# Kernel tuning notes

Hardware: AMD Instinct MI355X
Metric: run time of the kernel (lower is better)

## Reference

```python
import jax, jax.numpy as jnp
import numpy as np

B, S, DIM, H = 2, 2048, 2048, 16
HD = DIM // H  # head_dim = 128
EPS = 1e-6


def setup_inputs() -> dict:
    key = jax.random.key(0)
    ks = jax.random.split(key, 13)
    d = {
        'hidden_states': jax.random.normal(ks[0], (B, S, DIM), jnp.float32),
        'freqs_cos': jax.random.normal(ks[1], (1, S, 1, HD), jnp.float32),
        'freqs_sin': jax.random.normal(ks[2], (1, S, 1, HD), jnp.float32),
        'Wq': jax.random.normal(ks[3], (DIM, DIM), jnp.float32) * 0.02,
        'bq': jax.random.normal(ks[4], (DIM,), jnp.float32) * 0.02,
        'Wk': jax.random.normal(ks[5], (DIM, DIM), jnp.float32) * 0.02,
        'bk': jax.random.normal(ks[6], (DIM,), jnp.float32) * 0.02,
        'Wv': jax.random.normal(ks[7], (DIM, DIM), jnp.float32) * 0.02,
        'bv': jax.random.normal(ks[8], (DIM,), jnp.float32) * 0.02,
        'norm_q_w': jax.random.uniform(ks[9], (DIM,), jnp.float32, 0.5, 1.5),
        'norm_k_w': jax.random.uniform(ks[10], (DIM,), jnp.float32, 0.5, 1.5),
        'Wo': jax.random.normal(ks[11], (DIM, DIM), jnp.float32) * 0.02,
        'bo': jax.random.normal(ks[12], (DIM,), jnp.float32) * 0.02,
    }
    return d


def _rms_norm(x, w, eps=EPS):
    # local RMSNorm over the full inner_dim (no cross-rank reduce)
    xf = x.astype(jnp.float32)
    var = jnp.mean(xf * xf, axis=-1, keepdims=True)
    return (w * (xf * jax.lax.rsqrt(var + eps))).astype(x.dtype)


def _apply_rope(x, freqs_cos, freqs_sin):
    # x: [B,H,S,D]; freqs: [1,S,1,D] -> broadcast cos/sin at [1,1,S,D/2]
    dtype = x.dtype
    xf = x.astype(jnp.float32)
    x1 = xf[..., 0::2]
    x2 = xf[..., 1::2]
    cos = jnp.transpose(freqs_cos[..., 0::2], (0, 2, 1, 3)).astype(jnp.float32)
    sin = jnp.transpose(freqs_sin[..., 1::2], (0, 2, 1, 3)).astype(jnp.float32)
    even = x1 * cos - x2 * sin
    odd = x1 * sin + x2 * cos
    out = jnp.stack([even, odd], axis=-1).reshape(x.shape)
    return out.astype(dtype)


def reference(hidden_states, freqs_cos, freqs_sin, Wq, bq, Wk, bk, Wv, bv,
              norm_q_w, norm_k_w, Wo, bo):
    b, s, _ = hidden_states.shape
    q = hidden_states @ Wq.T + bq
    k = hidden_states @ Wk.T + bk
    v = hidden_states @ Wv.T + bv
    q = _rms_norm(q, norm_q_w)
    k = _rms_norm(k, norm_k_w)
    # [B,S,H*D] -> [B,H,S,D]
    q = q.reshape(b, s, H, HD).transpose(0, 2, 1, 3)
    k = k.reshape(b, s, H, HD).transpose(0, 2, 1, 3)
    v = v.reshape(b, s, H, HD).transpose(0, 2, 1, 3)
    q = _apply_rope(q, freqs_cos, freqs_sin)
    k = _apply_rope(k, freqs_cos, freqs_sin)
    # flash attention math (full, non-causal), scale = 1/sqrt(head_dim)
    scale = 1.0 / np.sqrt(HD).astype(np.float32)
    scores = jnp.einsum('bhqd,bhkd->bhqk', q, k) * scale
    attn = jax.nn.softmax(scores, axis=-1)
    out = jnp.einsum('bhqk,bhkd->bhqd', attn, v)
    out = out.transpose(0, 2, 1, 3).reshape(b, s, H * HD)
    return out @ Wo.T + bo
```

## Files before the change

kernel.cpp:

```cpp
#include <hip/hip_runtime.h>
#include <stdint.h>

#define DEVI __device__ __forceinline__

typedef __attribute__((ext_vector_type(8))) short bf16x8;
typedef __attribute__((ext_vector_type(4))) float f32x4;
typedef __attribute__((ext_vector_type(16))) float f32x16;
typedef __attribute__((ext_vector_type(4))) unsigned short u16x4;
typedef __attribute__((ext_vector_type(8))) unsigned short u16x8;

DEVI unsigned short f2bf(float f) {
    union { float f; unsigned u; } v; v.f = f;
    unsigned r = v.u + 0x7fffu + ((v.u >> 16) & 1u);
    return (unsigned short)(r >> 16);
}

DEVI float bf2f(unsigned short u) {
    union { unsigned u; float f; } v; v.u = ((unsigned)u) << 16;
    return v.f;
}

DEVI unsigned cvtpk(float lo, float hi) {
    unsigned r;
    asm("v_cvt_pk_bf16_f32 %0, %1, %2" : "=v"(r) : "v"(lo), "v"(hi));
    return r;
}

DEVI void gload16(const void* g, void* lds) {
    __builtin_amdgcn_global_load_lds(
        (const __attribute__((address_space(1))) unsigned int*)(uintptr_t)g,
        (__attribute__((address_space(3))) unsigned int*)(unsigned int)(uintptr_t)lds,
        16, 0, 0);
}

__global__ __launch_bounds__(256) void cvt_all(
    const float* __restrict__ hs, const float* __restrict__ wq,
    const float* __restrict__ wk, const float* __restrict__ wv,
    const float* __restrict__ wo,
    unsigned short* __restrict__ o_hs, unsigned short* __restrict__ o_wq,
    unsigned short* __restrict__ o_wk, unsigned short* __restrict__ o_wv,
    unsigned short* __restrict__ o_wo) {
    const int bid = blockIdx.x;
    const float* src; unsigned short* dst; int base;
    if (bid < 2048)      { src = hs; dst = o_hs; base = bid; }
    else if (bid < 3072) { src = wq; dst = o_wq; base = bid - 2048; }
    else if (bid < 4096) { src = wk; dst = o_wk; base = bid - 3072; }
    else if (bid < 5120) { src = wv; dst = o_wv; base = bid - 4096; }
    else                 { src = wo; dst = o_wo; base = bid - 5120; }
    const int i0 = base * 1024 + threadIdx.x;
#pragma unroll
    for (int k = 0; k < 4; k++) {
        const int i = i0 + k * 256;
        float4 v = ((const float4*)src)[i];
        u16x4 pk;
        pk[0] = f2bf(v.x); pk[1] = f2bf(v.y); pk[2] = f2bf(v.z); pk[3] = f2bf(v.w);
        ((u16x4*)dst)[i] = pk;
    }
}

DEVI void gemm_core256(const unsigned short* __restrict__ A,
                       const unsigned short* __restrict__ Wt,
                       int m0, int n0, char* lds,
                       f32x4 (&acc)[8][4]) {
    constexpr int K = 2048;
    const int t = threadIdx.x;
    const int w = t >> 6, l = t & 63, lr = l & 15, lk = l >> 4;
    const int wr = w >> 2, wc = w & 3;
    const int sx = lr & 7;
    const int srow = t >> 3, sseg = (t & 7) ^ (srow & 7);
    const unsigned short* aS = A + (size_t)(m0 + srow) * K + sseg * 8;
    const unsigned short* bS = Wt + (size_t)(n0 + srow) * K + sseg * 8;

#pragma unroll
    for (int mi = 0; mi < 8; mi++)
#pragma unroll
        for (int ni = 0; ni < 4; ni++) acc[mi][ni] = (f32x4){0.f, 0.f, 0.f, 0.f};

    auto STAGE = [&](int tt, int u) {
        if (tt >= 32) return;
        const int k0 = tt * 64, bb = tt & 1;
        if (u < 4)
            gload16(aS + (size_t)u * 64 * K + k0, lds + bb * 32768 + u * 8192 + w * 1024);
        else
            gload16(bS + (size_t)(u - 4) * 64 * K + k0,
                    lds + 65536 + bb * 32768 + (u - 4) * 8192 + w * 1024);
    };

    STAGE(0, 0); STAGE(0, 1); STAGE(0, 2); STAGE(0, 3);
    STAGE(0, 4); STAGE(0, 5); STAGE(0, 6); STAGE(0, 7);
    STAGE(1, 0); STAGE(1, 1); STAGE(1, 2); STAGE(1, 3);
    asm volatile("s_waitcnt vmcnt(4)" ::: "memory");
    __builtin_amdgcn_s_barrier();

    for (int kt = 0; kt < 32; ++kt) {
        const int bb = kt & 1;
        const char* Ab = lds + bb * 32768;
        const char* Bb = lds + 65536 + bb * 32768;
        bf16x8 a[8][2], b[4][2];
#pragma unroll
        for (int mi = 0; mi < 8; mi++)
#pragma unroll
            for (int ks = 0; ks < 2; ks++)
                a[mi][ks] = *(const bf16x8*)(Ab + (wr * 128 + mi * 16 + lr) * 128 +
                                             (((ks * 4 + lk) ^ sx) << 4));
#pragma unroll
        for (int ni = 0; ni < 4; ni++)
#pragma unroll
            for (int ks = 0; ks < 2; ks++)
                b[ni][ks] = *(const bf16x8*)(Bb + (wc * 64 + ni * 16 + lr) * 128 +
                                             (((ks * 4 + lk) ^ sx) << 4));
        STAGE(kt + 1, 4); STAGE(kt + 1, 5); STAGE(kt + 1, 6); STAGE(kt + 1, 7);
        __builtin_amdgcn_s_setprio(1);
#pragma unroll
        for (int mi = 0; mi < 8; mi++)
#pragma unroll
            for (int ni = 0; ni < 4; ni++)
                acc[mi][ni] = __builtin_amdgcn_mfma_f32_16x16x32_bf16(
                    a[mi][0], b[ni][0], acc[mi][ni], 0, 0, 0);
        __builtin_amdgcn_s_setprio(0);
        asm volatile("s_waitcnt lgkmcnt(0)" ::: "memory");
        __builtin_amdgcn_s_barrier();
        STAGE(kt + 2, 0); STAGE(kt + 2, 1); STAGE(kt + 2, 2); STAGE(kt + 2, 3);
        __builtin_amdgcn_s_setprio(1);
#pragma unroll
        for (int mi = 0; mi < 8; mi++)
#pragma unroll
            for (int ni = 0; ni < 4; ni++)
                acc[mi][ni] = __builtin_amdgcn_mfma_f32_16x16x32_bf16(
                    a[mi][1], b[ni][1], acc[mi][ni], 0, 0, 0);
        __builtin_amdgcn_s_setprio(0);
        if (kt < 30)       asm volatile("s_waitcnt vmcnt(4)" ::: "memory");
        else if (kt == 30) asm volatile("s_waitcnt vmcnt(0)" ::: "memory");
        __builtin_amdgcn_s_barrier();
    }
}

DEVI void gemm_pipe_core(const unsigned short* __restrict__ A,
                         const unsigned short* __restrict__ Wt,
                         int m0, int n0, char* lds,
                         f32x4 (&acc)[2][2][2][2]) {
    constexpr int K = 2048;
    const int t = threadIdx.x;
    const int w = t >> 6, l = t & 63, lr = l & 15, lk = l >> 4;
    const int wr = w >> 2, wc = w & 3;
    const int sx = lr & 7;
    const int srow = t >> 3, sseg = (t & 7) ^ (srow & 7);
    const unsigned short* aS = A + (size_t)(m0 + srow) * K + sseg * 8;
    const unsigned short* bS = Wt + (size_t)(n0 + srow) * K + sseg * 8;
    char* Bbase = lds + 32768;

#pragma unroll
    for (int qm = 0; qm < 2; qm++)
#pragma unroll
        for (int qn = 0; qn < 2; qn++)
#pragma unroll
            for (int fr = 0; fr < 2; fr++)
#pragma unroll
                for (int fc = 0; fc < 2; fc++)
                    acc[qm][qn][fr][fc] = (f32x4){0.f, 0.f, 0.f, 0.f};

    auto STAGE = [&](int tt, int u) {
        if (tt >= 32) return;
        const int k0 = tt * 64, bb = tt & 1;
        if (u < 4)
            gload16(bS + (size_t)u * 64 * K + k0, Bbase + bb * 32768 + u * 8192 + w * 1024);
        else
            gload16(aS + (size_t)(u - 4) * 64 * K + k0, lds + bb * 16384 + (u - 4) * 8192 + w * 1024);
    };

    STAGE(0, 0); STAGE(0, 1); STAGE(0, 2); STAGE(0, 3); STAGE(0, 4); STAGE(0, 5);
    STAGE(1, 0); STAGE(1, 1); STAGE(1, 2);
    asm volatile("s_waitcnt vmcnt(3)" ::: "memory");
    __builtin_amdgcn_s_barrier();

    for (int kt = 0; kt < 32; ++kt) {
        const int bb = kt & 1;
        const char* Ab = lds + bb * 16384;
        const char* Bb = Bbase + bb * 32768;
        bf16x8 a0[2][2], a1[2][2], b0[2][2], b1[2][2];
#pragma unroll
        for (int fr = 0; fr < 2; fr++)
#pragma unroll
            for (int ks = 0; ks < 2; ks++) {
                a0[fr][ks] = *(const bf16x8*)(Ab + (wr * 64 + fr * 16 + lr) * 128 +
                                              (((ks * 4 + lk) ^ sx) << 4));
                a1[fr][ks] = *(const bf16x8*)(Ab + (wr * 64 + 32 + fr * 16 + lr) * 128 +
                                              (((ks * 4 + lk) ^ sx) << 4));
            }
#pragma unroll
        for (int fc = 0; fc < 2; fc++)
#pragma unroll
            for (int ks = 0; ks < 2; ks++) {
                b0[fc][ks] = *(const bf16x8*)(Bb + (wc * 64 + fc * 16 + lr) * 128 +
                                              (((ks * 4 + lk) ^ sx) << 4));
                b1[fc][ks] = *(const bf16x8*)(Bb + (wc * 64 + 32 + fc * 16 + lr) * 128 +
                                              (((ks * 4 + lk) ^ sx) << 4));
            }
        STAGE(kt + 1, 3); STAGE(kt + 1, 4); STAGE(kt + 1, 5);
        __builtin_amdgcn_s_setprio(1);
#pragma unroll
        for (int ks = 0; ks < 2; ks++)
#pragma unroll
            for (int fr = 0; fr < 2; fr++)
#pragma unroll
                for (int fc = 0; fc < 2; fc++) {
                    acc[0][0][fr][fc] = __builtin_amdgcn_mfma_f32_16x16x32_bf16(
                        a0[fr][ks], b0[fc][ks], acc[0][0][fr][fc], 0, 0, 0);
                    acc[1][0][fr][fc] = __builtin_amdgcn_mfma_f32_16x16x32_bf16(
                        a1[fr][ks], b0[fc][ks], acc[1][0][fr][fc], 0, 0, 0);
                }
        __builtin_amdgcn_s_setprio(0);
        asm volatile("s_waitcnt lgkmcnt(0)" ::: "memory");
        __builtin_amdgcn_s_barrier();
        STAGE(kt + 2, 0); STAGE(kt + 2, 1); STAGE(kt + 2, 2);
        __builtin_amdgcn_s_setprio(1);
#pragma unroll
        for (int ks = 0; ks < 2; ks++)
#pragma unroll
            for (int fr = 0; fr < 2; fr++)
#pragma unroll
                for (int fc = 0; fc < 2; fc++) {
                    acc[0][1][fr][fc] = __builtin_amdgcn_mfma_f32_16x16x32_bf16(
                        a0[fr][ks], b1[fc][ks], acc[0][1][fr][fc], 0, 0, 0);
                    acc[1][1][fr][fc] = __builtin_amdgcn_mfma_f32_16x16x32_bf16(
                        a1[fr][ks], b1[fc][ks], acc[1][1][fr][fc], 0, 0, 0);
                }
        __builtin_amdgcn_s_setprio(0);
        if (kt < 30)       asm volatile("s_waitcnt vmcnt(3)" ::: "memory");
        else if (kt == 30) asm volatile("s_waitcnt vmcnt(0)" ::: "memory");
        __builtin_amdgcn_s_barrier();
    }
}

__global__ __launch_bounds__(512, 2) void gemm_qkv(
    const unsigned short* __restrict__ A,
    const unsigned short* __restrict__ Wq16, const unsigned short* __restrict__ Wk16,
    const unsigned short* __restrict__ Wv16,
    const float* __restrict__ bq, const float* __restrict__ bk, const float* __restrict__ bv,
    unsigned short* __restrict__ qh, unsigned short* __restrict__ kh,
    unsigned short* __restrict__ Vt) {
    __shared__ char Lds[131072];
    const int bid = blockIdx.x;
    const int nt = bid & 7, idx = bid >> 3;
    const int mt = idx & 15, z = idx >> 4;
    const int m0 = mt * 256, n0 = nt * 256;
    const unsigned short* W = (z == 0) ? Wq16 : (z == 1) ? Wk16 : Wv16;
    const float* bias = (z == 0) ? bq : (z == 1) ? bk : bv;

    f32x4 acc[8][4];
    gemm_core256(A, W, m0, n0, Lds, acc);

    const int t = threadIdx.x, w = t >> 6, l = t & 63, lr = l & 15, lk = l >> 4;
    const int wr = w >> 2, wc = w & 3;
#pragma unroll
    for (int mi = 0; mi < 8; mi++)
#pragma unroll
        for (int ni = 0; ni < 4; ni++) {
            const int col = n0 + wc * 64 + ni * 16 + lr;
            const int rb = m0 + wr * 128 + mi * 16 + lk * 4;
            const float bb = bias[col];
            if (z == 2) {
                const int hh = col >> 7, d = col & 127;
                const int b = rb >> 11, s = rb & 2047;
                u16x4 pk;
#pragma unroll
                for (int j = 0; j < 4; j++) pk[j] = f2bf(acc[mi][ni][j] + bb);
                *(u16x4*)(Vt + ((size_t)((b * 16 + hh) * 128 + d)) * 2048 + s) = pk;
            } else {
                unsigned short* out = (z == 0) ? qh : kh;
#pragma unroll
                for (int j = 0; j < 4; j++)
                    out[(size_t)(rb + j) * 2048 + col] = f2bf(acc[mi][ni][j] + bb);
            }
        }
}

__global__ __launch_bounds__(512, 2) void gemm_o(
    const unsigned short* __restrict__ A, const unsigned short* __restrict__ W16,
    const float* __restrict__ bo, float* __restrict__ out) {
    __shared__ char Lds[98304];
    const int bid = blockIdx.x;
    const int nt = bid & 7, mt = bid >> 3;
    const int m0 = mt * 128, n0 = nt * 256;

    f32x4 acc[2][2][2][2];
    gemm_pipe_core(A, W16, m0, n0, Lds, acc);

    const int t = threadIdx.x, w = t >> 6, l = t & 63, lr = l & 15, lk = l >> 4;
    const int wr = w >> 2, wc = w & 3;
#pragma unroll
    for (int qm = 0; qm < 2; qm++)
#pragma unroll
        for (int qn = 0; qn < 2; qn++)
#pragma unroll
            for (int fr = 0; fr < 2; fr++)
#pragma unroll
                for (int fc = 0; fc < 2; fc++) {
                    const int col = n0 + wc * 64 + qn * 32 + fc * 16 + lr;
                    const int rb = m0 + wr * 64 + qm * 32 + fr * 16 + lk * 4;
                    const float bb = bo[col];
#pragma unroll
                    for (int j = 0; j < 4; j++)
                        out[(size_t)(rb + j) * 2048 + col] = acc[qm][qn][fr][fc][j] + bb;
                }
}

__global__ __launch_bounds__(256) void norm_rope(
    const unsigned short* __restrict__ qh, const unsigned short* __restrict__ kh,
    const float* __restrict__ nqw, const float* __restrict__ nkw,
    const float* __restrict__ fc, const float* __restrict__ fs,
    unsigned short* __restrict__ Qr, unsigned short* __restrict__ Kr) {
    const int row = blockIdx.x;
    const int which = blockIdx.y;
    const unsigned short* in = which ? kh : qh;
    const float* wv = which ? nkw : nqw;
    unsigned short* out = which ? Kr : Qr;
    const float qs = which ? 1.0f : 0.12751744f;
    const int t = threadIdx.x;
    u16x8 xr = *(const u16x8*)(in + (size_t)row * 2048 + t * 8);
    float xv[8];
#pragma unroll
    for (int e = 0; e < 8; e++) xv[e] = bf2f(xr[e]);
    float ss = 0.f;
#pragma unroll
    for (int e = 0; e < 8; e++) ss += xv[e] * xv[e];
#pragma unroll
    for (int m = 1; m < 64; m <<= 1) ss += __shfl_xor(ss, m, 64);
    __shared__ float red[4];
    if ((t & 63) == 0) red[t >> 6] = ss;
    __syncthreads();
    const float tot = red[0] + red[1] + red[2] + red[3];
    const float r = rsqrtf(tot * (1.0f / 2048.0f) + 1e-6f);
    const int s = row & 2047, b = row >> 11;
    const int d0 = t * 8, hd0 = d0 & 127, h = d0 >> 7;
    float4 c0 = ((const float4*)(fc + s * 128 + hd0))[0];
    float4 c1 = ((const float4*)(fc + s * 128 + hd0))[1];
    float4 s0 = ((const float4*)(fs + s * 128 + hd0))[0];
    float4 s1 = ((const float4*)(fs + s * 128 + hd0))[1];
    float4 w0 = ((const float4*)(wv + d0))[0];
    float4 w1 = ((const float4*)(wv + d0))[1];
    float wn[8] = {w0.x, w0.y, w0.z, w0.w, w1.x, w1.y, w1.z, w1.w};
    float xn[8];
#pragma unroll
    for (int e = 0; e < 8; e++) xn[e] = xv[e] * wn[e] * r;
    float o[8];
    o[0] = xn[0] * c0.x - xn[1] * s0.y;  o[1] = xn[0] * s0.y + xn[1] * c0.x;
    o[2] = xn[2] * c0.z - xn[3] * s0.w;  o[3] = xn[2] * s0.w + xn[3] * c0.z;
    o[4] = xn[4] * c1.x - xn[5] * s1.y;  o[5] = xn[4] * s1.y + xn[5] * c1.x;
    o[6] = xn[6] * c1.z - xn[7] * s1.w;  o[7] = xn[6] * s1.w + xn[7] * c1.z;
    u16x8 pk;
#pragma unroll
    for (int e = 0; e < 8; e++) pk[e] = f2bf(o[e] * qs);
    *(u16x8*)(out + ((size_t)((b * 16 + h) * 2048 + s)) * 128 + hd0) = pk;
}

__global__ __launch_bounds__(256, 2) void attn(
    const unsigned short* __restrict__ Qr, const unsigned short* __restrict__ Kr,
    const unsigned short* __restrict__ Vt, unsigned short* __restrict__ Ao) {
    __shared__ unsigned short Kl[2][64 * 128];
    __shared__ unsigned short Vl[2][128 * 64];
    const int t = threadIdx.x, w = t >> 6, l = t & 63;
    const int ql = l & 31, h = l >> 5;
    const int bid = blockIdx.x;
    const int xcd = bid & 7, idx = bid >> 3;
    const int bh = xcd * 4 + (idx >> 4);
    const int q0 = (idx & 15) * 128 + w * 32;
    const int b = bh >> 4, head = bh & 15;

    const unsigned short* Qp = Qr + ((size_t)bh * 2048 + q0) * 128;
    bf16x8 qf[8];
#pragma unroll
    for (int c8 = 0; c8 < 8; c8++)
        qf[c8] = *(const bf16x8*)(Qp + ql * 128 + c8 * 16 + h * 8);

    f32x16 accO[4];
#pragma unroll
    for (int dt = 0; dt < 4; dt++)
#pragma unroll
        for (int r = 0; r < 16; r++) accO[dt][r] = 0.f;
    float mj = -1e30f, ljp = 0.f;

    const unsigned short* Kb = Kr + (size_t)bh * 2048 * 128;
    const unsigned short* Vb = Vt + (size_t)bh * 128 * 2048;
    const int krow = t >> 4, kseg = (t & 15) ^ (krow & 7);
    const int vrow = t >> 3, vseg = (t & 7) ^ (vrow & 7);

    auto STAGE = [&](int buf, int kv0) {
        char* kd = (char*)&Kl[buf][0] + w * 1024;
        char* vd = (char*)&Vl[buf][0] + w * 1024;
#pragma unroll
        for (int c = 0; c < 4; c++)
            gload16(Kb + (size_t)(kv0 + c * 16 + krow) * 128 + kseg * 8, kd + c * 4096);
#pragma unroll
        for (int c = 0; c < 4; c++)
            gload16(Vb + (size_t)(c * 32 + vrow) * 2048 + kv0 + vseg * 8, vd + c * 4096);
    };

    const int qx = ql & 7;
    STAGE(0, 0);
    __syncthreads();
    int cur = 0;
    for (int it = 0; it < 32; ++it) {
        if (it < 31) STAGE(cur ^ 1, (it + 1) * 64);
        f32x16 S0, S1;
#pragma unroll
        for (int r = 0; r < 16; r++) { S0[r] = 0.f; S1[r] = 0.f; }
        __builtin_amdgcn_s_setprio(1);
#pragma unroll
        for (int c8 = 0; c8 < 8; c8++) {
            const int sg = ((c8 * 2 + h) ^ qx) << 4;
            bf16x8 k0 = *(const bf16x8*)((const char*)&Kl[cur][0] + ql * 256 + sg);
            bf16x8 k1 = *(const bf16x8*)((const char*)&Kl[cur][0] + (32 + ql) * 256 + sg);
            S0 = __builtin_amdgcn_mfma_f32_32x32x16_bf16(k0, qf[c8], S0, 0, 0, 0);
            S1 = __builtin_amdgcn_mfma_f32_32x32x16_bf16(k1, qf[c8], S1, 0, 0, 0);
        }
        __builtin_amdgcn_s_setprio(0);
        float mloc = S0[0];
#pragma unroll
        for (int r = 1; r < 16; r++) mloc = fmaxf(mloc, S0[r]);
#pragma unroll
        for (int r = 0; r < 16; r++) mloc = fmaxf(mloc, S1[r]);
        const float mx = fmaxf(mloc, __shfl_xor(mloc, 32, 64));
        if (!__all(mx <= mj + 8.0f)) {
            const float mn = fmaxf(mj, mx);
            const float corr = exp2f(mj - mn);
            mj = mn;
            ljp *= corr;
#pragma unroll
            for (int dt = 0; dt < 4; dt++)
#pragma unroll
                for (int r = 0; r < 16; r++) accO[dt][r] *= corr;
        }
        unsigned W[16];
        float lsum = 0.f;
#pragma unroll
        for (int i = 0; i < 8; i++) {
            const float pa = exp2f(S0[2 * i] - mj);
            const float pb = exp2f(S0[2 * i + 1] - mj);
            W[i] = cvtpk(pa, pb);
            lsum += pa + pb;
        }
#pragma unroll
        for (int i = 0; i < 8; i++) {
            const float pa = exp2f(S1[2 * i] - mj);
            const float pb = exp2f(S1[2 * i + 1] - mj);
            W[8 + i] = cvtpk(pa, pb);
            lsum += pa + pb;
        }
        ljp += lsum;
#pragma unroll
        for (int c = 0; c < 2; c++) {
            unsigned X[8];
#pragma unroll
            for (int i = 0; i < 8; i++)
                X[i] = (unsigned)__shfl_xor((int)W[c * 8 + i], 32, 64);
            union U { unsigned u[4]; bf16x8 v; };
            U F, G;
            F.u[0] = h ? X[2] : W[c * 8 + 0];
            F.u[1] = h ? X[3] : W[c * 8 + 1];
            F.u[2] = h ? W[c * 8 + 2] : X[0];
            F.u[3] = h ? W[c * 8 + 3] : X[1];
            G.u[0] = h ? X[6] : W[c * 8 + 4];
            G.u[1] = h ? X[7] : W[c * 8 + 5];
            G.u[2] = h ? W[c * 8 + 6] : X[4];
            G.u[3] = h ? W[c * 8 + 7] : X[5];
            __builtin_amdgcn_s_setprio(1);
#pragma unroll
            for (int dt = 0; dt < 4; dt++) {
                const int sg = (((2 * c) * 2 + h) ^ qx) << 4;
                bf16x8 vf = *(const bf16x8*)((const char*)&Vl[cur][0] + (dt * 32 + ql) * 128 + sg);
                accO[dt] = __builtin_amdgcn_mfma_f32_32x32x16_bf16(vf, F.v, accO[dt], 0, 0, 0);
            }
#pragma unroll
            for (int dt = 0; dt < 4; dt++) {
                const int sg = (((2 * c + 1) * 2 + h) ^ qx) << 4;
                bf16x8 vf = *(const bf16x8*)((const char*)&Vl[cur][0] + (dt * 32 + ql) * 128 + sg);
                accO[dt] = __builtin_amdgcn_mfma_f32_32x32x16_bf16(vf, G.v, accO[dt], 0, 0, 0);
            }
            __builtin_amdgcn_s_setprio(0);
        }
        __syncthreads();
        cur ^= 1;
    }
    const float lj = ljp + __shfl_xor(ljp, 32, 64);
    const float inv = 1.0f / lj;
    unsigned short* ob = Ao + ((size_t)(b * 2048 + q0 + ql)) * 2048 + head * 128;
#pragma unroll
    for (int dt = 0; dt < 4; dt++)
#pragma unroll
        for (int i = 0; i < 8; i++) {
            const float a = accO[dt][2 * i] * inv;
            const float c = accO[dt][2 * i + 1] * inv;
            const int d = dt * 32 + ((2 * i) & 3) + 8 * (i >> 1) + 4 * h;
            *(unsigned*)(ob + d) = cvtpk(a, c);
        }
}

extern "C" void kernel_launch(void* const* d_in, const int* in_sizes, int n_in,
                              void* d_out, int out_size, void* d_ws, size_t ws_size,
                              hipStream_t stream) {
    const float* hs  = (const float*)d_in[0];
    const float* fc  = (const float*)d_in[1];
    const float* fs  = (const float*)d_in[2];
    const float* Wq  = (const float*)d_in[3];
    const float* bq  = (const float*)d_in[4];
    const float* Wk  = (const float*)d_in[5];
    const float* bk  = (const float*)d_in[6];
    const float* Wv  = (const float*)d_in[7];
    const float* bv  = (const float*)d_in[8];
    const float* nqw = (const float*)d_in[9];
    const float* nkw = (const float*)d_in[10];
    const float* Wo  = (const float*)d_in[11];
    const float* bo  = (const float*)d_in[12];
    float* out = (float*)d_out;

    char* p = (char*)d_ws;
    unsigned short* hs16 = (unsigned short*)p; p += (size_t)8388608 * 2;
    unsigned short* Wq16 = (unsigned short*)p; p += (size_t)4194304 * 2;
    unsigned short* Wk16 = (unsigned short*)p; p += (size_t)4194304 * 2;
    unsigned short* Wv16 = (unsigned short*)p; p += (size_t)4194304 * 2;
    unsigned short* Wo16 = (unsigned short*)p; p += (size_t)4194304 * 2;
    unsigned short* qh = (unsigned short*)p;   p += (size_t)8388608 * 2;
    unsigned short* kh = (unsigned short*)p;   p += (size_t)8388608 * 2;
    unsigned short* Qr = (unsigned short*)p;   p += (size_t)8388608 * 2;
    unsigned short* Kr = (unsigned short*)p;   p += (size_t)8388608 * 2;
    unsigned short* Vt = (unsigned short*)p;   p += (size_t)8388608 * 2;
    unsigned short* Ao = (unsigned short*)p;   p += (size_t)8388608 * 2;
    (void)ws_size; (void)in_sizes; (void)n_in; (void)out_size;

    cvt_all<<<6144, 256, 0, stream>>>(hs, Wq, Wk, Wv, Wo,
                                      hs16, Wq16, Wk16, Wv16, Wo16);
    gemm_qkv<<<384, 512, 0, stream>>>(hs16, Wq16, Wk16, Wv16,
                                      bq, bk, bv, qh, kh, Vt);
    norm_rope<<<dim3(4096, 2), 256, 0, stream>>>(qh, kh, nqw, nkw, fc, fs, Qr, Kr);
    attn<<<512, 256, 0, stream>>>(Qr, Kr, Vt, Ao);
    gemm_o<<<256, 512, 0, stream>>>(Ao, Wo16, bo, out);
}
```

Baseline: 298.5 us.

## Split QKV GEMM main loop into eight-phase interleaved load/MFMA schedule

Restructures the 256x256 QKV GEMM K-loop into four sub-phases per tile. Each phase loads a slice of A fragments, issues one half of the next A or B tile's global-to-LDS copies, and runs the matching MFMA block. B becomes the operand prefetched two tiles ahead instead of A. The goal is to overlap LDS reads, global prefetch and MFMA more finely and to hold fewer A fragments in registers. The cost is more barriers per tile, which adds synchronisation overhead and hazard risk.

New measurement: 304.4 us. Within noise of the previous version (+2.0%).

```diff
diff --git a/kernel.cpp b/kernel.cpp
--- a/kernel.cpp
+++ b/kernel.cpp
@@ -58,11 +58,11 @@
     }
 }
 
-DEVI void gemm_core256(const unsigned short* __restrict__ A,
-                       const unsigned short* __restrict__ Wt,
-                       int m0, int n0, char* lds,
-                       f32x4 (&acc)[8][4]) {
-    constexpr int K = 2048;
+DEVI void gemm_core256_8ph(const unsigned short* __restrict__ A,
+                           const unsigned short* __restrict__ Wt,
+                           int m0, int n0, char* lds,
+                           f32x4 (&acc)[8][4]) {
+    constexpr int K = 2048, NT = 32;
     const int t = threadIdx.x;
     const int w = t >> 6, l = t & 63, lr = l & 15, lk = l >> 4;
     const int wr = w >> 2, wc = w & 3;
@@ -76,62 +76,72 @@
 #pragma unroll
         for (int ni = 0; ni < 4; ni++) acc[mi][ni] = (f32x4){0.f, 0.f, 0.f, 0.f};
 
-    auto STAGE = [&](int tt, int u) {
-        if (tt >= 32) return;
+    auto STAGE_A = [&](int tt, int half) {
+        if (tt >= NT) return;
         const int k0 = tt * 64, bb = tt & 1;
-        if (u < 4)
-            gload16(aS + (size_t)u * 64 * K + k0, lds + bb * 32768 + u * 8192 + w * 1024);
-        else
-            gload16(bS + (size_t)(u - 4) * 64 * K + k0,
-                    lds + 65536 + bb * 32768 + (u - 4) * 8192 + w * 1024);
+        char* d = lds + bb * 32768 + half * 16384 + w * 1024;
+        gload16(aS + (size_t)(half * 128) * K + k0, d);
+        gload16(aS + (size_t)(half * 128 + 64) * K + k0, d + 8192);
     };
-
-    STAGE(0, 0); STAGE(0, 1); STAGE(0, 2); STAGE(0, 3);
-    STAGE(0, 4); STAGE(0, 5); STAGE(0, 6); STAGE(0, 7);
-    STAGE(1, 0); STAGE(1, 1); STAGE(1, 2); STAGE(1, 3);
+    auto STAGE_B = [&](int tt, int half) {
+        if (tt >= NT) return;
+        const int k0 = tt * 64, bb = tt & 1;
+        char* d = lds + 65536 + bb * 32768 + half * 16384 + w * 1024;
+        gload16(bS + (size_t)(half * 128) * K + k0, d);
+        gload16(bS + (size_t)(half * 128 + 64) * K + k0, d + 8192);
+    };
+
+    STAGE_A(0, 0); STAGE_A(0, 1);
+    STAGE_B(0, 0); STAGE_B(0, 1);
+    STAGE_B(1, 0); STAGE_B(1, 1);
     asm volatile("s_waitcnt vmcnt(4)" ::: "memory");
     __builtin_amdgcn_s_barrier();
 
-    for (int kt = 0; kt < 32; ++kt) {
+    for (int kt = 0; kt < NT; ++kt) {
         const int bb = kt & 1;
         const char* Ab = lds + bb * 32768;
         const char* Bb = lds + 65536 + bb * 32768;
-        bf16x8 a[8][2], b[4][2];
-#pragma unroll
-        for (int mi = 0; mi < 8; mi++)
+        bf16x8 b[4][2];
+#pragma unroll
+        for (int p = 0; p < 4; ++p) {
+            bf16x8 a[2][2];
+            if (p == 0) {
+#pragma unroll
+                for (int ni = 0; ni < 4; ni++)
+#pragma unroll
+                    for (int ks = 0; ks < 2; ks++)
+                        b[ni][ks] = *(const bf16x8*)(Bb + (wc * 64 + ni * 16 + lr) * 128 +
+                                                     (((ks * 4 + lk) ^ sx) << 4));
+            }
+#pragma unroll
+            for (int mi = 0; mi < 2; mi++)
+#pragma unroll
+                for (int ks = 0; ks < 2; ks++)
+                    a[mi][ks] = *(const bf16x8*)(Ab + (wr * 128 + (2 * p + mi) * 16 + lr) * 128 +
+                                                 (((ks * 4 + lk) ^ sx) << 4));
+            if (p == 0)      STAGE_A(kt + 1, 0);
+            else if (p == 1) STAGE_A(kt + 1, 1);
+            else if (p == 2) STAGE_B(kt + 2, 0);
+            else             STAGE_B(kt + 2, 1);
+            if (p == 0) asm volatile("s_waitcnt lgkmcnt(8)" ::: "memory");
+            __builtin_amdgcn_s_barrier();
+            asm volatile("s_waitcnt lgkmcnt(0)" ::: "memory");
+            __builtin_amdgcn_s_setprio(1);
 #pragma unroll
             for (int ks = 0; ks < 2; ks++)
-                a[mi][ks] = *(const bf16x8*)(Ab + (wr * 128 + mi * 16 + lr) * 128 +
-                                             (((ks * 4 + lk) ^ sx) << 4));
-#pragma unroll
-        for (int ni = 0; ni < 4; ni++)
-#pragma unroll
-            for (int ks = 0; ks < 2; ks++)
-                b[ni][ks] = *(const bf16x8*)(Bb + (wc * 64 + ni * 16 + lr) * 128 +
-                                             (((ks * 4 + lk) ^ sx) << 4));
-        STAGE(kt + 1, 4); STAGE(kt + 1, 5); STAGE(kt + 1, 6); STAGE(kt + 1, 7);
-        __builtin_amdgcn_s_setprio(1);
-#pragma unroll
-        for (int mi = 0; mi < 8; mi++)
-#pragma unroll
-            for (int ni = 0; ni < 4; ni++)
-                acc[mi][ni] = __builtin_amdgcn_mfma_f32_16x16x32_bf16(
-                    a[mi][0], b[ni][0], acc[mi][ni], 0, 0, 0);
-        __builtin_amdgcn_s_setprio(0);
-        asm volatile("s_waitcnt lgkmcnt(0)" ::: "memory");
-        __builtin_amdgcn_s_barrier();
-        STAGE(kt + 2, 0); STAGE(kt + 2, 1); STAGE(kt + 2, 2); STAGE(kt + 2, 3);
-        __builtin_amdgcn_s_setprio(1);
-#pragma unroll
-        for (int mi = 0; mi < 8; mi++)
-#pragma unroll
-            for (int ni = 0; ni < 4; ni++)
-                acc[mi][ni] = __builtin_amdgcn_mfma_f32_16x16x32_bf16(
-                    a[mi][1], b[ni][1], acc[mi][ni], 0, 0, 0);
-        __builtin_amdgcn_s_setprio(0);
-        if (kt < 30)       asm volatile("s_waitcnt vmcnt(4)" ::: "memory");
-        else if (kt == 30) asm volatile("s_waitcnt vmcnt(0)" ::: "memory");
-        __builtin_amdgcn_s_barrier();
+#pragma unroll
+                for (int mi = 0; mi < 2; mi++)
+#pragma unroll
+                    for (int ni = 0; ni < 4; ni++)
+                        acc[2 * p + mi][ni] = __builtin_amdgcn_mfma_f32_16x16x32_bf16(
+                            a[mi][ks], b[ni][ks], acc[2 * p + mi][ni], 0, 0, 0);
+            __builtin_amdgcn_s_setprio(0);
+            if (p == 3) {
+                if (kt < 30)       asm volatile("s_waitcnt vmcnt(4)" ::: "memory");
+                else if (kt == 30) asm volatile("s_waitcnt vmcnt(0)" ::: "memory");
+            }
+            __builtin_amdgcn_s_barrier();
+        }
     }
 }
 
@@ -248,7 +258,7 @@
     const float* bias = (z == 0) ? bq : (z == 1) ? bk : bv;
 
     f32x4 acc[8][4];
-    gemm_core256(A, W, m0, n0, Lds, acc);
+    gemm_core256_8ph(A, W, m0, n0, Lds, acc);
 
     const int t = threadIdx.x, w = t >> 6, l = t & 63, lr = l & 15, lk = l >> 4;
     const int wr = w >> 2, wc = w & 3;
```
